# Kernel optimization log

Measured on AMD Instinct MI355X. Metric: run time of the kernel, lower is better.

The kernel has to match this reference:

```python
import jax, jax.numpy as jnp
import numpy as np


def setup_inputs() -> dict:
    key = jax.random.key(0)
    k1, k2 = jax.random.split(key)
    N, T, D = 65536, 128, 2
    source = jax.random.normal(k1, (N, T, D), dtype=jnp.float32)
    mask = jax.random.randint(k2, (N, T, D), 0, 2).astype(jnp.float32)
    # Fixed (non-trainable) inertia-model matrices, as in the torch module.
    A = jnp.array([[0.0, 0.0, -1.0, 0.0],
                   [0.0, 0.0, 0.0, -1.0],
                   [0.0, 0.0, 0.0, 0.0],
                   [0.0, 0.0, 0.0, 0.0]], dtype=jnp.float32)
    B = jnp.array([[1.0, 0.0, 1.0, 0.0],
                   [0.0, 1.0, 0.0, 1.0]], dtype=jnp.float32)
    C = jnp.array([[0.0, 0.0],
                   [0.0, 0.0],
                   [1.0, 0.0],
                   [0.0, 1.0]], dtype=jnp.float32)
    return {"source": source, "mask": mask, "A": A, "B": B, "C": C,
            "burn_in_steps": 64}


def reference(source, mask, A, B, C, burn_in_steps):
    # use_mask=True variant of the Inertia model.
    N, T, D = source.shape
    state_dim = 4
    burn_in = int(burn_in_steps)

    src_t = jnp.swapaxes(source, 0, 1)  # [T, N, D]
    msk_t = jnp.swapaxes(mask, 0, 1)    # [T, N, D]
    ts = jnp.arange(T)

    s0 = jnp.zeros((N, state_dim), dtype=source.dtype)
    m0 = jnp.zeros((N, D), dtype=source.dtype)
    y0 = jnp.zeros((N, D), dtype=source.dtype)  # never used on first step

    def step(carry, inp):
        s, m, y = carry
        x_t, mask_t, t = inp
        in_burn = (burn_in <= 0) | (t < burn_in)  # scalar bool
        m_prev = m
        m_new = jnp.where(in_burn, mask_t, m)     # mask only advances in burn-in
        s_app = (1.0 - m_prev) * m_new            # [N, 2]
        x = jnp.where(in_burn, x_t, y)
        s_temp = s @ A + x @ B                    # [N, 4]
        s_next = jnp.concatenate(
            [s_temp[:, :2],
             s[:, 2:4] * s_app + s_temp[:, 2:4] * (1.0 - s_app)], axis=1)
        del_x = s_next @ C                        # [N, 2]
        y_new = x + del_x
        return (s_next, m_new, y_new), y_new

    _, pred = jax.lax.scan(step, (s0, m0, y0), (src_t, msk_t, ts))
    return jnp.swapaxes(pred, 0, 1)  # [N, T, D]
```

## Files before the change

kernel.cpp:

```cpp
#include <hip/hip_runtime.h>


#define SEQ_F4 64
#define BURN_F4 32

__global__ __launch_bounds__(256) void inertia_fused(
    const float* __restrict__ src, const float* __restrict__ msk,
    float* __restrict__ out, int nseq)
{
    const int n = blockIdx.x * blockDim.x + threadIdx.x;
    if (n >= nseq) return;
    const size_t row = (size_t)n * 256;
    const float4* __restrict__ s4 = (const float4*)(src + row);
    const float4* __restrict__ m4 = (const float4*)(msk + row);
    float4* __restrict__ o4 = (float4*)(out + row);

    float p0=0.f, p1=0.f;
    float q0=0.f, q1=0.f;
    float mm0=0.f, mm1=0.f;
    float y0=0.f, y1=0.f;

    constexpr int PF = 4;
    float4 sb[PF], mb[PF];
#pragma unroll
    for (int i = 0; i < PF; ++i) { sb[i] = s4[i]; mb[i] = m4[i]; }

#pragma unroll
    for (int i = 0; i < BURN_F4; ++i) {
        float4 sv = sb[i & (PF - 1)];
        float4 mv = mb[i & (PF - 1)];
        if (i + PF < BURN_F4) {
            sb[i & (PF - 1)] = s4[i + PF];
            mb[i & (PF - 1)] = m4[i + PF];
        }
        float a0 = (1.f - mm0) * mv.x;
        float a1 = (1.f - mm1) * mv.y;
        q0 = q0 * a0 + (sv.x - p0) * (1.f - a0);
        q1 = q1 * a1 + (sv.y - p1) * (1.f - a1);
        float ya0 = sv.x + q0, ya1 = sv.y + q1;
        p0 = sv.x; p1 = sv.y; mm0 = mv.x; mm1 = mv.y;
        a0 = (1.f - mm0) * mv.z;
        a1 = (1.f - mm1) * mv.w;
        q0 = q0 * a0 + (sv.z - p0) * (1.f - a0);
        q1 = q1 * a1 + (sv.w - p1) * (1.f - a1);
        y0 = sv.z + q0; y1 = sv.w + q1;
        p0 = sv.z; p1 = sv.w; mm0 = mv.z; mm1 = mv.w;
        o4[i] = make_float4(ya0, ya1, y0, y1);
    }

    float a0 = (1.f - mm0) * mm0;
    float a1 = (1.f - mm1) * mm1;
    float d0 = q0 * a0 + (y0 - p0) * (1.f - a0);
    float d1 = q1 * a1 + (y1 - p1) * (1.f - a1);
    float cy0 = y0 + d0, cy1 = y1 + d1;

#pragma unroll
    for (int j = 0; j < 32; ++j) {
        o4[BURN_F4 + j] = make_float4(cy0, cy1, cy0 + d0, cy1 + d1);
        cy0 += 2.f * d0; cy1 += 2.f * d1;
    }
}

extern "C" void kernel_launch(void* const* d_in, const int* in_sizes, int n_in,
                              void* d_out, int out_size, void* d_ws, size_t ws_size,
                              hipStream_t stream) {
    const float* src = (const float*)d_in[0];
    const float* msk = (const float*)d_in[1];
    float* out = (float*)d_out;
    const int nseq = in_sizes[0] / 256;
    const int block = 256;
    const int grid = (nseq + block - 1) / block;
    inertia_fused<<<grid, block, 0, stream>>>(src, msk, out, nseq);
}
```

Measured before the change: 191.6 us.

## Parallelize per-sequence recurrence as wavefront shuffle scan with coalesced loads

Assigns one 64-lane wavefront per sequence instead of one thread, computing the burn-in linear recurrence via a log-step shuffle-based associative scan. Each lane loads and stores one float2 so global memory accesses become coalesced, and the autoregressive tail is written as a linear extrapolation from the last lane's state. This removes strided per-thread access and serial dependency chains at the cost of extra shuffle and multiply work and hardcodes the 64-step burn-in layout.

```diff
diff --git a/kernel.cpp b/kernel.cpp
--- a/kernel.cpp
+++ b/kernel.cpp
@@ -1,64 +1,57 @@
 #include <hip/hip_runtime.h>
 
 
-#define SEQ_F4 64
-#define BURN_F4 32
-
-__global__ __launch_bounds__(256) void inertia_fused(
+__global__ __launch_bounds__(256) void inertia_scan(
     const float* __restrict__ src, const float* __restrict__ msk,
     float* __restrict__ out, int nseq)
 {
-    const int n = blockIdx.x * blockDim.x + threadIdx.x;
+    const int n = (blockIdx.x * 256 + threadIdx.x) >> 6;
+    const int lane = threadIdx.x & 63;
     if (n >= nseq) return;
-    const size_t row = (size_t)n * 256;
-    const float4* __restrict__ s4 = (const float4*)(src + row);
-    const float4* __restrict__ m4 = (const float4*)(msk + row);
-    float4* __restrict__ o4 = (float4*)(out + row);
+    const size_t base = (size_t)n * 128;
+    const float2* __restrict__ s2 = (const float2*)src + base;
+    const float2* __restrict__ m2 = (const float2*)msk + base;
+    float2* __restrict__ o2 = (float2*)out + base;
 
-    float p0=0.f, p1=0.f;
-    float q0=0.f, q1=0.f;
-    float mm0=0.f, mm1=0.f;
-    float y0=0.f, y1=0.f;
+    float2 sv = s2[lane];
+    float2 mv = m2[lane];
 
-    constexpr int PF = 4;
-    float4 sb[PF], mb[PF];
-#pragma unroll
-    for (int i = 0; i < PF; ++i) { sb[i] = s4[i]; mb[i] = m4[i]; }
+    float spx = __shfl_up(sv.x, 1, 64);
+    float spy = __shfl_up(sv.y, 1, 64);
+    float mpx = __shfl_up(mv.x, 1, 64);
+    float mpy = __shfl_up(mv.y, 1, 64);
+    const bool l0 = (lane == 0);
+    spx = l0 ? 0.f : spx;  spy = l0 ? 0.f : spy;
+    mpx = l0 ? 0.f : mpx;  mpy = l0 ? 0.f : mpy;
+
+    float A0 = (1.f - mpx) * mv.x;
+    float A1 = (1.f - mpy) * mv.y;
+    float B0 = (sv.x - spx) * (1.f - A0);
+    float B1 = (sv.y - spy) * (1.f - A1);
 
 #pragma unroll
-    for (int i = 0; i < BURN_F4; ++i) {
-        float4 sv = sb[i & (PF - 1)];
-        float4 mv = mb[i & (PF - 1)];
-        if (i + PF < BURN_F4) {
-            sb[i & (PF - 1)] = s4[i + PF];
-            mb[i & (PF - 1)] = m4[i + PF];
-        }
-        float a0 = (1.f - mm0) * mv.x;
-        float a1 = (1.f - mm1) * mv.y;
-        q0 = q0 * a0 + (sv.x - p0) * (1.f - a0);
-        q1 = q1 * a1 + (sv.y - p1) * (1.f - a1);
-        float ya0 = sv.x + q0, ya1 = sv.y + q1;
-        p0 = sv.x; p1 = sv.y; mm0 = mv.x; mm1 = mv.y;
-        a0 = (1.f - mm0) * mv.z;
-        a1 = (1.f - mm1) * mv.w;
-        q0 = q0 * a0 + (sv.z - p0) * (1.f - a0);
-        q1 = q1 * a1 + (sv.w - p1) * (1.f - a1);
-        y0 = sv.z + q0; y1 = sv.w + q1;
-        p0 = sv.z; p1 = sv.w; mm0 = mv.z; mm1 = mv.w;
-        o4[i] = make_float4(ya0, ya1, y0, y1);
+    for (int off = 1; off < 64; off <<= 1) {
+        float Ap0 = __shfl_up(A0, off, 64);
+        float Bp0 = __shfl_up(B0, off, 64);
+        float Ap1 = __shfl_up(A1, off, 64);
+        float Bp1 = __shfl_up(B1, off, 64);
+        const bool act = (lane >= off);
+        Ap0 = act ? Ap0 : 1.f;  Bp0 = act ? Bp0 : 0.f;
+        Ap1 = act ? Ap1 : 1.f;  Bp1 = act ? Bp1 : 0.f;
+        B0 = fmaf(Bp0, A0, B0);  A0 *= Ap0;
+        B1 = fmaf(Bp1, A1, B1);  A1 *= Ap1;
     }
 
-    float a0 = (1.f - mm0) * mm0;
-    float a1 = (1.f - mm1) * mm1;
-    float d0 = q0 * a0 + (y0 - p0) * (1.f - a0);
-    float d1 = q1 * a1 + (y1 - p1) * (1.f - a1);
-    float cy0 = y0 + d0, cy1 = y1 + d1;
+    const float y0 = sv.x + B0;
+    const float y1 = sv.y + B1;
+    o2[lane] = make_float2(y0, y1);
 
-#pragma unroll
-    for (int j = 0; j < 32; ++j) {
-        o4[BURN_F4 + j] = make_float4(cy0, cy1, cy0 + d0, cy1 + d1);
-        cy0 += 2.f * d0; cy1 += 2.f * d1;
-    }
+    const float q63x = __shfl(B0, 63, 64);
+    const float q63y = __shfl(B1, 63, 64);
+    const float y63x = __shfl(y0, 63, 64);
+    const float y63y = __shfl(y1, 63, 64);
+    const float tj = (float)(lane + 1);
+    o2[64 + lane] = make_float2(fmaf(tj, q63x, y63x), fmaf(tj, q63y, y63y));
 }
 
 extern "C" void kernel_launch(void* const* d_in, const int* in_sizes, int n_in,
@@ -69,6 +62,6 @@
     float* out = (float*)d_out;
     const int nseq = in_sizes[0] / 256;
     const int block = 256;
-    const int grid = (nseq + block - 1) / block;
-    inertia_fused<<<grid, block, 0, stream>>>(src, msk, out, nseq);
+    const int grid = (nseq + 3) / 4;
+    inertia_scan<<<grid, block, 0, stream>>>(src, msk, out, nseq);
 }
```

Result: faster. 160.3 us (-16.3%).
